# Performance work log

Measured on AMD Instinct MI355X. Metric: run time of the kernel, lower is better.

## Reference

```python
import jax, jax.numpy as jnp
import numpy as np

B, Lq, Lkv = 4, 1024, 4096
Cq, Ckv, E, NH = 512, 512, 512, 8
HD = E // NH


def setup_inputs() -> dict:
    key = jax.random.key(0)
    ks = jax.random.split(key, 8)
    s = 0.02
    return {
        "Xq": jax.random.normal(ks[0], (B, Lq, Cq), dtype=jnp.float32),
        "Xkv": jax.random.normal(ks[1], (B, Lkv, Ckv), dtype=jnp.float32),
        "mask": jax.random.randint(ks[2], (B, Lq, 1), 0, 2, dtype=jnp.int32),
        "Wq": jax.random.normal(ks[3], (Cq, E), dtype=jnp.float32) * s,
        "bq": jnp.zeros((E,), dtype=jnp.float32),
        "Wkv": jax.random.normal(ks[4], (Ckv, 2 * E), dtype=jnp.float32) * s,
        "bkv": jnp.zeros((2 * E,), dtype=jnp.float32),
        "Wp": jax.random.normal(ks[5], (E, E), dtype=jnp.float32) * s,
        "bp": jnp.zeros((E,), dtype=jnp.float32),
        "attn_pos": jax.random.normal(ks[6], (1, NH, Lq, Lkv), dtype=jnp.float32) * s,
    }


def reference(Xq, Xkv, mask, Wq, bq, Wkv, bkv, Wp, bp, attn_pos):
    scale = HD ** -0.5
    # projections
    Q = (Xq @ Wq + bq).reshape(B, Lq, NH, HD).transpose(0, 2, 1, 3) * scale  # [B,NH,Lq,HD]
    KV = (Xkv @ Wkv + bkv).reshape(B, Lkv, 2, NH, HD)
    K = KV[:, :, 0].transpose(0, 2, 1, 3)  # [B,NH,Lkv,HD]
    V = KV[:, :, 1].transpose(0, 2, 1, 3)
    # scores + learned positional bias
    attn = jnp.einsum('bhqd,bhkd->bhqk', Q, K) + attn_pos  # [B,NH,Lq,Lkv]
    # dummy-column masked softmax (mask: [B,Lq,1], 1=keep row)
    m = mask.astype(attn.dtype)[:, None]           # [B,1,Lq,1]
    attn = attn + (1.0 - m) * (-100.0)             # suppress masked query rows
    dummy = jnp.broadcast_to(jnp.where(m == 0, 100.0, -100.0), (B, NH, Lq, 1))
    attn = jax.nn.softmax(jnp.concatenate([attn, dummy], axis=-1), axis=-1)[..., :Lkv]
    # weighted sum + output projection (dropout = identity in eval)
    out = jnp.einsum('bhqk,bhkd->bhqd', attn, V)
    out = out.transpose(0, 2, 1, 3).reshape(B, Lq, E)
    return out @ Wp + bp
```

## Files before the change

### kernel.cpp

```cpp
#include <hip/hip_runtime.h>

typedef unsigned short u16;
typedef __attribute__((ext_vector_type(8))) short bf16x8;
typedef __attribute__((ext_vector_type(4))) float f32x4;
typedef __attribute__((ext_vector_type(2))) unsigned u32x2;
typedef __attribute__((ext_vector_type(4))) unsigned u32x4;

__device__ __forceinline__ u16 f2bf(float x) {
    union { float f; unsigned u; } v; v.f = x;
    unsigned r = v.u + 0x7FFF + ((v.u >> 16) & 1);
    return (u16)(r >> 16);
}

__device__ __forceinline__ unsigned cvt_pk_bf16(float lo, float hi) {
    unsigned r;
    asm("v_cvt_pk_bf16_f32 %0, %1, %2" : "=v"(r) : "v"(lo), "v"(hi));
    return r;
}

__device__ __forceinline__ bf16x8 pk8(const f32x4& s0, const f32x4& s1) {
    union { u32x4 u; bf16x8 v; } x;
    x.u[0] = cvt_pk_bf16(s0[0], s0[1]);
    x.u[1] = cvt_pk_bf16(s0[2], s0[3]);
    x.u[2] = cvt_pk_bf16(s1[0], s1[1]);
    x.u[3] = cvt_pk_bf16(s1[2], s1[3]);
    return x.v;
}

__device__ __forceinline__ void gl_lds16(const u16* g, u16* l) {
    __builtin_amdgcn_global_load_lds((const __attribute__((address_space(1))) void*)g,
                                     (__attribute__((address_space(3))) void*)l, 16, 0, 0);
}

__global__ __launch_bounds__(256) void conv_bf16(const float* __restrict__ in,
                                                 u16* __restrict__ out) {
    size_t i = ((size_t)blockIdx.x * 256 + threadIdx.x) * 8;
    const float4* p = (const float4*)(in + i);
    float4 a = p[0], b = p[1];
    u32x4 w = {cvt_pk_bf16(a.x, a.y), cvt_pk_bf16(a.z, a.w),
               cvt_pk_bf16(b.x, b.y), cvt_pk_bf16(b.z, b.w)};
    *(u32x4*)(out + i) = w;
}

__global__ __launch_bounds__(256) void transpose_w(const float* __restrict__ in,
                                                   u16* __restrict__ out, int R, int C) {
    __shared__ float tile[64][65];
    int r0 = blockIdx.y * 64, c0 = blockIdx.x * 64;
    int tid = threadIdx.x;
#pragma unroll
    for (int j = 0; j < 16; ++j) {
        int e = tid + j * 256;
        int row = e >> 6, col = e & 63;
        tile[row][col] = in[(size_t)(r0 + row) * C + c0 + col];
    }
    __syncthreads();
#pragma unroll
    for (int j = 0; j < 16; ++j) {
        int e = tid + j * 256;
        int row = e >> 6, col = e & 63;
        out[(size_t)(c0 + row) * R + r0 + col] = f2bf(tile[col][row]);
    }
}

__global__ __launch_bounds__(256) void transpose_v(const u16* __restrict__ in,
                                                   u16* __restrict__ out) {
    __shared__ u16 tile[64][65];
    int bh = blockIdx.y;
    int r0 = blockIdx.x * 64;
    const u16* ip = in + (size_t)bh * 4096 * 64;
    u16* op = out + (size_t)bh * 64 * 4096;
    int tid = threadIdx.x;
#pragma unroll
    for (int j = 0; j < 16; ++j) {
        int e = tid + j * 256;
        int row = e >> 6, col = e & 63;
        tile[row][col] = ip[(size_t)(r0 + row) * 64 + col];
    }
    __syncthreads();
#pragma unroll
    for (int j = 0; j < 16; ++j) {
        int e = tid + j * 256;
        int row = e >> 6, col = e & 63;
        int c5 = col & 31;
        int src = (col & 32) | ((((c5 >> 2) & 1) << 4) + ((c5 >> 3) << 2) + (c5 & 3));
        op[(size_t)row * 4096 + r0 + col] = tile[src][row];
    }
}

template <int MODE>
__global__ __launch_bounds__(256) void gemm_kernel(const u16* __restrict__ A,
                                                   const u16* __restrict__ Bt,
                                                   const float* __restrict__ bias,
                                                   void* __restrict__ Cout,
                                                   void* __restrict__ Cout2,
                                                   int M, int N, int K) {
    __shared__ u16 Al[128][64];
    __shared__ u16 Bl[128][64];
    int tid = threadIdx.x;
    int lane = tid & 63, wid = tid >> 6;
    int wr = wid >> 1, wc = wid & 1;
    int l15 = lane & 15, g = lane >> 4;
    int bm = blockIdx.y, bn = blockIdx.x;
    int ldr = lane >> 3, ldc = (lane & 7) << 3;

    f32x4 acc[4][4];
#pragma unroll
    for (int m = 0; m < 4; ++m)
#pragma unroll
        for (int n = 0; n < 4; ++n)
#pragma unroll
            for (int j = 0; j < 4; ++j) acc[m][n][j] = 0.f;

    int nK = K >> 6;
    for (int kt = 0; kt < nK; ++kt) {
        __syncthreads();
#pragma unroll
        for (int i = 0; i < 4; ++i) {
            int c = wid * 4 + i;
            int row = c * 8 + ldr;
            gl_lds16(A + (size_t)(bm * 128 + row) * K + kt * 64 + ldc, &Al[0][0] + c * 512);
            gl_lds16(Bt + (size_t)(bn * 128 + row) * K + kt * 64 + ldc, &Bl[0][0] + c * 512);
        }
        __syncthreads();

#pragma unroll
        for (int kk = 0; kk < 2; ++kk) {
            bf16x8 af[4], bfr[4];
#pragma unroll
            for (int m = 0; m < 4; ++m)
                af[m] = *(const bf16x8*)&Al[wr * 64 + m * 16 + l15][kk * 32 + g * 8];
#pragma unroll
            for (int n = 0; n < 4; ++n)
                bfr[n] = *(const bf16x8*)&Bl[wc * 64 + n * 16 + l15][kk * 32 + g * 8];
#pragma unroll
            for (int m = 0; m < 4; ++m)
#pragma unroll
                for (int n = 0; n < 4; ++n)
                    acc[m][n] =
                        __builtin_amdgcn_mfma_f32_16x16x32_bf16(af[m], bfr[n], acc[m][n], 0, 0, 0);
        }
    }

#pragma unroll
    for (int m = 0; m < 4; ++m)
#pragma unroll
        for (int n = 0; n < 4; ++n)
#pragma unroll
            for (int j = 0; j < 4; ++j) {
                int row = bm * 128 + wr * 64 + m * 16 + g * 4 + j;
                int col = bn * 128 + wc * 64 + n * 16 + l15;
                float v = acc[m][n][j] + bias[col];
                if (MODE == 0) {
                    int b = row >> 10, q = row & 1023, h = col >> 6, d = col & 63;
                    ((u16*)Cout)[(((size_t)((b * 8 + h) * 1024 + q)) << 6) + d] =
                        f2bf(v * 0.18033688011112042f);
                } else if (MODE == 1) {
                    int b = row >> 12, kv = row & 4095;
                    int d = col & 63;
                    if (col < 512) {
                        int h = col >> 6;
                        ((u16*)Cout)[(((size_t)((b * 8 + h) * 4096 + kv)) << 6) + d] = f2bf(v);
                    } else {
                        int h = (col - 512) >> 6;
                        ((u16*)Cout2)[(((size_t)((b * 8 + h) * 4096 + kv)) << 6) + d] = f2bf(v);
                    }
                } else {
                    ((float*)Cout)[(size_t)row * N + col] = v;
                }
            }
}

__global__ __launch_bounds__(256, 2) void attn_kernel(const u16* __restrict__ Qb,
                                                      const u16* __restrict__ Kb,
                                                      const u16* __restrict__ Vt,
                                                      const float* __restrict__ pos,
                                                      float* __restrict__ Opart,
                                                      float* __restrict__ Lp) {
    __shared__ u16 Kl[2][4][2048];
    __shared__ u16 Vl[2][4][2048];

    int idx = blockIdx.x;
    int h = idx & 7;
    int rest = idx >> 3;
    int qt = rest & 15, sp = rest >> 4;
    int q0 = qt * 64;
    int kvb = sp * 1024;
    int tid = threadIdx.x, lane = tid & 63, wid = tid >> 6;
    int l15 = lane & 15, g = lane >> 4;

    const u16* Kg = Kb + ((size_t)(wid * 8 + h)) * (4096 * 64);
    const u16* Vg = Vt + ((size_t)(wid * 8 + h)) * (4096 * 64);
    int lr = lane >> 3;
    int swc = ((lane & 7) ^ lr) << 3;
    int sx = l15 & 7;

    bf16x8 aq[4][2];
#pragma unroll
    for (int b = 0; b < 4; ++b) {
        const u16* qp =
            Qb + (((size_t)((b * 8 + h) * 1024 + q0 + wid * 16 + l15)) << 6) + g * 8;
        aq[b][0] = *(const bf16x8*)(qp);
        aq[b][1] = *(const bf16x8*)(qp + 32);
    }

    f32x4 o[4][4];
    f32x4 lacc[4];
#pragma unroll
    for (int b = 0; b < 4; ++b) {
#pragma unroll
        for (int j = 0; j < 4; ++j) lacc[b][j] = 0.f;
#pragma unroll
        for (int n = 0; n < 4; ++n)
#pragma unroll
            for (int j = 0; j < 4; ++j) o[b][n][j] = 0.f;
    }

    auto STAGE = [&](int buf, int ktile) {
        int kv0 = kvb + ktile * 32;
#pragma unroll
        for (int c = 0; c < 4; ++c) {
            gl_lds16(Kg + (size_t)(kv0 + c * 8 + lr) * 64 + swc, &Kl[buf][wid][c * 512]);
            gl_lds16(Vg + (size_t)lane * 4096 + kv0 + c * 8, &Vl[buf][wid][c * 512]);
        }
    };

    const float* pp =
        pos + (size_t)h * 4194304 + (size_t)(q0 + wid * 16 + l15) * 4096 + kvb + g * 4;

    const short one_s = (short)0x3F80;
    bf16x8 ones = {one_s, one_s, one_s, one_s, one_s, one_s, one_s, one_s};

    STAGE(0, 0);
    f32x4 zr[2];
#pragma unroll
    for (int n = 0; n < 2; ++n) {
        zr[n] = *(const f32x4*)(pp + n * 16);
#pragma unroll
        for (int j = 0; j < 4; ++j) zr[n][j] *= 1.44269504f;
    }

    for (int kt = 0; kt < 32; ++kt) {
        int cur = kt & 1;
        __syncthreads();
        if (kt < 31) STAGE(cur ^ 1, kt + 1);

        int kn = (kt + 1) & 31;
        f32x4 zn0 = *(const f32x4*)(pp + kn * 32);
        f32x4 zn1 = *(const f32x4*)(pp + kn * 32 + 16);

#pragma unroll
        for (int b = 0; b < 4; ++b) {
            const u16* Kc = &Kl[cur][b][0];
            const u16* Vc = &Vl[cur][b][0];

            bf16x8 kb[2][2], vb[4];
#pragma unroll
            for (int n = 0; n < 2; ++n) {
                const u16* krow = Kc + (n * 16 + l15) * 64;
                kb[n][0] = *(const bf16x8*)(krow + ((g ^ sx) << 3));
                kb[n][1] = *(const bf16x8*)(krow + (((4 + g) ^ sx) << 3));
            }
#pragma unroll
            for (int n = 0; n < 4; ++n)
                vb[n] = *(const bf16x8*)(Vc + g * 512 + (n * 16 + l15) * 8);

            f32x4 s[2];
            __builtin_amdgcn_s_setprio(1);
#pragma unroll
            for (int n = 0; n < 2; ++n) {
                f32x4 t =
                    __builtin_amdgcn_mfma_f32_16x16x32_bf16(kb[n][0], aq[b][0], zr[n], 0, 0, 0);
                s[n] = __builtin_amdgcn_mfma_f32_16x16x32_bf16(kb[n][1], aq[b][1], t, 0, 0, 0);
            }
            __builtin_amdgcn_s_setprio(0);

#pragma unroll
            for (int n = 0; n < 2; ++n)
#pragma unroll
                for (int j = 0; j < 4; ++j)
                    s[n][j] = __builtin_exp2f(fminf(s[n][j], 80.f));

            bf16x8 pa = pk8(s[0], s[1]);

            __builtin_amdgcn_s_setprio(1);
#pragma unroll
            for (int n = 0; n < 4; ++n)
                o[b][n] = __builtin_amdgcn_mfma_f32_16x16x32_bf16(pa, vb[n], o[b][n], 0, 0, 0);
            lacc[b] = __builtin_amdgcn_mfma_f32_16x16x32_bf16(pa, ones, lacc[b], 0, 0, 0);
            __builtin_amdgcn_s_setprio(0);
        }

#pragma unroll
        for (int j = 0; j < 4; ++j) {
            zr[0][j] = zn0[j] * 1.44269504f;
            zr[1][j] = zn1[j] * 1.44269504f;
        }
    }

#pragma unroll
    for (int b = 0; b < 4; ++b) {
        int obase = (sp * 32 + b * 8 + h) * 1024;
#pragma unroll
        for (int j = 0; j < 4; ++j) {
            int row = q0 + wid * 16 + g * 4 + j;
#pragma unroll
            for (int n = 0; n < 4; ++n)
                __builtin_nontemporal_store(o[b][n][j],
                                            &Opart[((size_t)(obase + row)) * 64 + n * 16 + l15]);
            if (l15 == 0) __builtin_nontemporal_store(lacc[b][j], &Lp[obase + row]);
        }
    }
}

__global__ __launch_bounds__(256) void attn_combine(const float* __restrict__ Opart,
                                                    const float* __restrict__ Lp,
                                                    const int* __restrict__ mask,
                                                    u16* __restrict__ AO) {
    int tid = threadIdx.x;
    int d = tid & 63;
    int r = blockIdx.x * 4 + (tid >> 6);
    int bh = r >> 10, q = r & 1023;
    int b = bh >> 3, h = bh & 7;

    float L = 0.f, val = 0.f;
#pragma unroll
    for (int s2 = 0; s2 < 4; ++s2) {
        size_t rr = (size_t)(s2 * 32 + bh) * 1024 + q;
        L += Lp[rr];
        val += Opart[rr * 64 + d];
    }
    float res = mask[b * 1024 + q] ? (val / L) : 0.f;
    AO[((size_t)(b * 1024 + q)) * 512 + h * 64 + d] = f2bf(res);
}

extern "C" void kernel_launch(void* const* d_in, const int* in_sizes, int n_in,
                              void* d_out, int out_size, void* d_ws, size_t ws_size,
                              hipStream_t stream) {
    const float* Xq = (const float*)d_in[0];
    const float* Xkv = (const float*)d_in[1];
    const int* mask = (const int*)d_in[2];
    const float* Wq = (const float*)d_in[3];
    const float* bq = (const float*)d_in[4];
    const float* Wkv = (const float*)d_in[5];
    const float* bkv = (const float*)d_in[6];
    const float* Wp = (const float*)d_in[7];
    const float* bp = (const float*)d_in[8];
    const float* pos = (const float*)d_in[9];
    float* out = (float*)d_out;

    char* ws = (char*)d_ws;
    u16* WqT = (u16*)(ws);
    u16* WkvT = (u16*)(ws + 524288);
    u16* WpT = (u16*)(ws + 1572864);
    u16* Qb = (u16*)(ws + 2097152);
    u16* Kb = (u16*)(ws + 6291456);
    u16* Vt = (u16*)(ws + 23068672);
    u16* AO = (u16*)(ws + 39845888);
    float* Opart = (float*)(ws + 44040192);
    u16* Xkvb = (u16*)(ws + 44040192);
    u16* Vtm = (u16*)(ws + 60817408);
    u16* Xqb = (u16*)(ws + 77594624);
    float* Lp = (float*)(ws + 111149056);

    conv_bf16<<<dim3(1024), 256, 0, stream>>>(Xq, Xqb);
    conv_bf16<<<dim3(4096), 256, 0, stream>>>(Xkv, Xkvb);
    transpose_w<<<dim3(8, 8), 256, 0, stream>>>(Wq, WqT, 512, 512);
    transpose_w<<<dim3(16, 8), 256, 0, stream>>>(Wkv, WkvT, 512, 1024);
    transpose_w<<<dim3(8, 8), 256, 0, stream>>>(Wp, WpT, 512, 512);
    gemm_kernel<0><<<dim3(4, 32), 256, 0, stream>>>(Xqb, WqT, bq, Qb, nullptr, 4096, 512, 512);
    gemm_kernel<1><<<dim3(8, 128), 256, 0, stream>>>(Xkvb, WkvT, bkv, Kb, Vtm, 16384, 1024, 512);
    transpose_v<<<dim3(64, 32), 256, 0, stream>>>(Vtm, Vt);
    attn_kernel<<<dim3(512), 256, 0, stream>>>(Qb, Kb, Vt, pos, Opart, Lp);
    attn_combine<<<dim3(8192), 256, 0, stream>>>(Opart, Lp, mask, AO);
    gemm_kernel<2><<<dim3(4, 32), 256, 0, stream>>>(AO, WpT, bp, out, nullptr, 4096, 512, 512);
}
```

Before: 205.1 us.

## Split attention blocks over batch pairs to double grid and occupancy

Each attention block now handles two batches instead of four, so the grid doubles to 1024 blocks and launch bounds allow four blocks per CU with half the LDS. The staging is rewritten so two waves load K and two load V rather than every wave loading both. The fminf clamp before exp2 is dropped and the V fragment loads move after the softmax, with a sched_barrier placed before staging. The trade-off is that the attn_pos bias tile is now read by twice as many blocks, and removing the clamp relies on scores staying in range.

After: 192.4 us. 6.2% less time.

```diff
diff --git a/kernel.cpp b/kernel.cpp
--- a/kernel.cpp
+++ b/kernel.cpp
@@ -170,57 +170,65 @@
             }
 }
 
-__global__ __launch_bounds__(256, 2) void attn_kernel(const u16* __restrict__ Qb,
+__global__ __launch_bounds__(256, 4) void attn_kernel(const u16* __restrict__ Qb,
                                                       const u16* __restrict__ Kb,
                                                       const u16* __restrict__ Vt,
                                                       const float* __restrict__ pos,
                                                       float* __restrict__ Opart,
                                                       float* __restrict__ Lp) {
-    __shared__ u16 Kl[2][4][2048];
-    __shared__ u16 Vl[2][4][2048];
+    __shared__ u16 Kl[2][2][2048];
+    __shared__ u16 Vl[2][2][2048];
 
     int idx = blockIdx.x;
     int h = idx & 7;
     int rest = idx >> 3;
+    int bp = rest & 1;
+    rest >>= 1;
     int qt = rest & 15, sp = rest >> 4;
     int q0 = qt * 64;
     int kvb = sp * 1024;
     int tid = threadIdx.x, lane = tid & 63, wid = tid >> 6;
     int l15 = lane & 15, g = lane >> 4;
 
-    const u16* Kg = Kb + ((size_t)(wid * 8 + h)) * (4096 * 64);
-    const u16* Vg = Vt + ((size_t)(wid * 8 + h)) * (4096 * 64);
+    int sb = wid & 1;
+    bool stK = wid < 2;
+    const u16* SG =
+        (stK ? Kb : Vt) + ((size_t)((bp * 2 + sb) * 8 + h)) * (4096 * 64);
     int lr = lane >> 3;
     int swc = ((lane & 7) ^ lr) << 3;
     int sx = l15 & 7;
 
-    bf16x8 aq[4][2];
-#pragma unroll
-    for (int b = 0; b < 4; ++b) {
+    bf16x8 aq[2][2];
+#pragma unroll
+    for (int bi = 0; bi < 2; ++bi) {
         const u16* qp =
-            Qb + (((size_t)((b * 8 + h) * 1024 + q0 + wid * 16 + l15)) << 6) + g * 8;
-        aq[b][0] = *(const bf16x8*)(qp);
-        aq[b][1] = *(const bf16x8*)(qp + 32);
-    }
-
-    f32x4 o[4][4];
-    f32x4 lacc[4];
-#pragma unroll
-    for (int b = 0; b < 4; ++b) {
-#pragma unroll
-        for (int j = 0; j < 4; ++j) lacc[b][j] = 0.f;
+            Qb + (((size_t)(((bp * 2 + bi) * 8 + h) * 1024 + q0 + wid * 16 + l15)) << 6) + g * 8;
+        aq[bi][0] = *(const bf16x8*)(qp);
+        aq[bi][1] = *(const bf16x8*)(qp + 32);
+    }
+
+    f32x4 o[2][4];
+    f32x4 lacc[2];
+#pragma unroll
+    for (int bi = 0; bi < 2; ++bi) {
+#pragma unroll
+        for (int j = 0; j < 4; ++j) lacc[bi][j] = 0.f;
 #pragma unroll
         for (int n = 0; n < 4; ++n)
 #pragma unroll
-            for (int j = 0; j < 4; ++j) o[b][n][j] = 0.f;
+            for (int j = 0; j < 4; ++j) o[bi][n][j] = 0.f;
     }
 
     auto STAGE = [&](int buf, int ktile) {
         int kv0 = kvb + ktile * 32;
-#pragma unroll
-        for (int c = 0; c < 4; ++c) {
-            gl_lds16(Kg + (size_t)(kv0 + c * 8 + lr) * 64 + swc, &Kl[buf][wid][c * 512]);
-            gl_lds16(Vg + (size_t)lane * 4096 + kv0 + c * 8, &Vl[buf][wid][c * 512]);
+        if (stK) {
+#pragma unroll
+            for (int c = 0; c < 4; ++c)
+                gl_lds16(SG + (size_t)(kv0 + c * 8 + lr) * 64 + swc, &Kl[buf][sb][c * 512]);
+        } else {
+#pragma unroll
+            for (int c = 0; c < 4; ++c)
+                gl_lds16(SG + (size_t)lane * 4096 + kv0 + c * 8, &Vl[buf][sb][c * 512]);
         }
     };
 
@@ -242,51 +250,53 @@
     for (int kt = 0; kt < 32; ++kt) {
         int cur = kt & 1;
         __syncthreads();
-        if (kt < 31) STAGE(cur ^ 1, kt + 1);
 
         int kn = (kt + 1) & 31;
         f32x4 zn0 = *(const f32x4*)(pp + kn * 32);
         f32x4 zn1 = *(const f32x4*)(pp + kn * 32 + 16);
-
-#pragma unroll
-        for (int b = 0; b < 4; ++b) {
-            const u16* Kc = &Kl[cur][b][0];
-            const u16* Vc = &Vl[cur][b][0];
-
-            bf16x8 kb[2][2], vb[4];
+        __builtin_amdgcn_sched_barrier(0);
+        if (kt < 31) STAGE(cur ^ 1, kt + 1);
+
+#pragma unroll
+        for (int bi = 0; bi < 2; ++bi) {
+            const u16* Kc = &Kl[cur][bi][0];
+            const u16* Vc = &Vl[cur][bi][0];
+
+            bf16x8 kb[2][2];
 #pragma unroll
             for (int n = 0; n < 2; ++n) {
                 const u16* krow = Kc + (n * 16 + l15) * 64;
                 kb[n][0] = *(const bf16x8*)(krow + ((g ^ sx) << 3));
                 kb[n][1] = *(const bf16x8*)(krow + (((4 + g) ^ sx) << 3));
             }
+
+            f32x4 s[2];
+            __builtin_amdgcn_s_setprio(1);
+#pragma unroll
+            for (int n = 0; n < 2; ++n) {
+                f32x4 t =
+                    __builtin_amdgcn_mfma_f32_16x16x32_bf16(kb[n][0], aq[bi][0], zr[n], 0, 0, 0);
+                s[n] = __builtin_amdgcn_mfma_f32_16x16x32_bf16(kb[n][1], aq[bi][1], t, 0, 0, 0);
+            }
+            __builtin_amdgcn_s_setprio(0);
+
+#pragma unroll
+            for (int n = 0; n < 2; ++n)
+#pragma unroll
+                for (int j = 0; j < 4; ++j) s[n][j] = __builtin_exp2f(s[n][j]);
+
+            bf16x8 pa = pk8(s[0], s[1]);
+
+            bf16x8 vb[4];
 #pragma unroll
             for (int n = 0; n < 4; ++n)
                 vb[n] = *(const bf16x8*)(Vc + g * 512 + (n * 16 + l15) * 8);
 
-            f32x4 s[2];
             __builtin_amdgcn_s_setprio(1);
 #pragma unroll
-            for (int n = 0; n < 2; ++n) {
-                f32x4 t =
-                    __builtin_amdgcn_mfma_f32_16x16x32_bf16(kb[n][0], aq[b][0], zr[n], 0, 0, 0);
-                s[n] = __builtin_amdgcn_mfma_f32_16x16x32_bf16(kb[n][1], aq[b][1], t, 0, 0, 0);
-            }
-            __builtin_amdgcn_s_setprio(0);
-
-#pragma unroll
-            for (int n = 0; n < 2; ++n)
-#pragma unroll
-                for (int j = 0; j < 4; ++j)
-                    s[n][j] = __builtin_exp2f(fminf(s[n][j], 80.f));
-
-            bf16x8 pa = pk8(s[0], s[1]);
-
-            __builtin_amdgcn_s_setprio(1);
-#pragma unroll
             for (int n = 0; n < 4; ++n)
-                o[b][n] = __builtin_amdgcn_mfma_f32_16x16x32_bf16(pa, vb[n], o[b][n], 0, 0, 0);
-            lacc[b] = __builtin_amdgcn_mfma_f32_16x16x32_bf16(pa, ones, lacc[b], 0, 0, 0);
+                o[bi][n] = __builtin_amdgcn_mfma_f32_16x16x32_bf16(pa, vb[n], o[bi][n], 0, 0, 0);
+            lacc[bi] = __builtin_amdgcn_mfma_f32_16x16x32_bf16(pa, ones, lacc[bi], 0, 0, 0);
             __builtin_amdgcn_s_setprio(0);
         }
 
@@ -298,16 +308,16 @@
     }
 
 #pragma unroll
-    for (int b = 0; b < 4; ++b) {
-        int obase = (sp * 32 + b * 8 + h) * 1024;
+    for (int bi = 0; bi < 2; ++bi) {
+        int obase = (sp * 32 + (bp * 2 + bi) * 8 + h) * 1024;
 #pragma unroll
         for (int j = 0; j < 4; ++j) {
             int row = q0 + wid * 16 + g * 4 + j;
 #pragma unroll
             for (int n = 0; n < 4; ++n)
-                __builtin_nontemporal_store(o[b][n][j],
+                __builtin_nontemporal_store(o[bi][n][j],
                                             &Opart[((size_t)(obase + row)) * 64 + n * 16 + l15]);
-            if (l15 == 0) __builtin_nontemporal_store(lacc[b][j], &Lp[obase + row]);
+            if (l15 == 0) __builtin_nontemporal_store(lacc[bi][j], &Lp[obase + row]);
         }
     }
 }
@@ -370,7 +380,7 @@
     gemm_kernel<0><<<dim3(4, 32), 256, 0, stream>>>(Xqb, WqT, bq, Qb, nullptr, 4096, 512, 512);
     gemm_kernel<1><<<dim3(8, 128), 256, 0, stream>>>(Xkvb, WkvT, bkv, Kb, Vtm, 16384, 1024, 512);
     transpose_v<<<dim3(64, 32), 256, 0, stream>>>(Vtm, Vt);
-    attn_kernel<<<dim3(512), 256, 0, stream>>>(Qb, Kb, Vt, pos, Opart, Lp);
+    attn_kernel<<<dim3(1024), 256, 0, stream>>>(Qb, Kb, Vt, pos, Opart, Lp);
     attn_combine<<<dim3(8192), 256, 0, stream>>>(Opart, Lp, mask, AO);
     gemm_kernel<2><<<dim3(4, 32), 256, 0, stream>>>(AO, WpT, bp, out, nullptr, 4096, 512, 512);
 }
```
